# Kernel optimization log

Measured on AMD Instinct MI355X. Metric: run time of the kernel, lower is better.

## Reference

```python
import jax, jax.numpy as jnp
import numpy as np

N_NODES = 100000


def setup_inputs() -> dict:
    key = jax.random.key(0)
    ks = jax.random.split(key, 6)
    x = jax.random.normal(ks[0], (N_NODES, 3), dtype=jnp.float32)
    edge_index = jax.random.randint(ks[1], (2, 1600000), 0, N_NODES, dtype=jnp.int32)
    W1 = jax.random.normal(ks[2], (6, 64), dtype=jnp.float32) * 0.2
    b1 = jnp.zeros((64,), dtype=jnp.float32)
    W2 = jax.random.normal(ks[3], (67, 128), dtype=jnp.float32) * 0.1
    b2 = jnp.zeros((128,), dtype=jnp.float32)
    Wc = jax.random.normal(ks[4], (128, 5), dtype=jnp.float32) * 0.1
    bc = jnp.zeros((5,), dtype=jnp.float32)
    return {"x": x, "edge_index": edge_index, "W1": W1, "b1": b1,
            "W2": W2, "b2": b2, "Wc": Wc, "bc": bc}


def _pointnet_conv(h, rel, src, dst, W, b, n):
    # gather neighbor features, MLP on [h_j, pos_j - pos_i], max-aggregate per node
    msg = jnp.concatenate([h[src], rel], axis=-1) @ W + b  # [E, out]
    agg = jax.ops.segment_max(msg, dst, num_segments=n)    # [N, out]
    return jax.nn.relu(agg)  # relu also maps -inf (isolated nodes) to 0


def reference(x, edge_index, W1, b1, W2, b2, Wc, bc):
    src, dst = edge_index[0], edge_index[1]
    pos = x  # forward uses data.x for both x and pos
    rel = pos[src] - pos[dst]                       # [E, 3]
    h = _pointnet_conv(x, rel, src, dst, W1, b1, N_NODES)   # [N, 64]
    h = _pointnet_conv(h, rel, src, dst, W2, b2, N_NODES)   # [N, 128]
    logits = h @ Wc + bc                            # [N, 5]
    return jax.nn.log_softmax(logits, axis=-1)
```

## Files before the change

### kernel.cpp

```cpp
#include <hip/hip_runtime.h>
#include <cstdint>

#define CAP 56
#define NBITS 7
#define BINSZ 128
#define BIN_CAP 2816
#define TILE_E 4096
#define SCANN 1024
#define EPT (TILE_E/256)

typedef _Float16 h2 __attribute__((ext_vector_type(2)));
typedef _Float16 h4 __attribute__((ext_vector_type(4)));
typedef _Float16 h8 __attribute__((ext_vector_type(8)));
typedef float f32x4 __attribute__((ext_vector_type(4)));

static __device__ inline h8 pkmax8(h8 a, h8 b) {
#if __has_builtin(__builtin_elementwise_max)
    return __builtin_elementwise_max(a, b);
#else
    h8 r;
    #pragma unroll
    for (int i = 0; i < 8; i += 2) {
        h2 aa = { a[i], a[i+1] }, bb = { b[i], b[i+1] }, rr;
        asm("v_pk_max_f16 %0, %1, %2" : "=v"(rr) : "v"(aa), "v"(bb));
        r[i] = rr.x; r[i+1] = rr.y;
    }
    return r;
#endif
}

__global__ __launch_bounds__(256) void xpack_kernel(
    const float* __restrict__ x, float4* __restrict__ xp,
    int* __restrict__ bin_cnt, int N)
{
    int n = blockIdx.x * 256 + threadIdx.x;
    if (n < N) xp[n] = make_float4(x[n*3], x[n*3+1], x[n*3+2], 0.f);
    if (blockIdx.x == 0) {
        #pragma unroll
        for (int j = 0; j < 4; ++j) bin_cnt[threadIdx.x + j * 256] = 0;
    }
}

__global__ __launch_bounds__(256) void bin_kernel(
    const int* __restrict__ ei, int* __restrict__ bin_cnt,
    int* __restrict__ pairs, int E, int nbins)
{
    __shared__ int hist[SCANN];
    __shared__ int sc[SCANN];
    __shared__ int gbase[SCANN];
    __shared__ int lofs[SCANN];
    __shared__ int words[TILE_E];
    __shared__ unsigned short binOf[TILE_E];
    int t = threadIdx.x;
    for (int i = t; i < SCANN; i += 256) { hist[i] = 0; lofs[i] = 0; }
    __syncthreads();
    int e0 = blockIdx.x * TILE_E;
    int s[EPT], d[EPT];
    #pragma unroll
    for (int i = 0; i < EPT; ++i) {
        int e = e0 + t + i * 256;
        bool ok = e < E;
        s[i] = ok ? ei[e] : 0;
        d[i] = ok ? ei[E + e] : -1;
        if (ok) atomicAdd(&hist[d[i] >> NBITS], 1);
    }
    __syncthreads();
    for (int i = t; i < SCANN; i += 256) sc[i] = hist[i];
    __syncthreads();
    for (int off = 1; off < SCANN; off <<= 1) {
        int v[4];
        #pragma unroll
        for (int j = 0; j < 4; ++j) {
            int i = t + j * 256;
            v[j] = (i >= off) ? sc[i - off] : 0;
        }
        __syncthreads();
        #pragma unroll
        for (int j = 0; j < 4; ++j) sc[t + j * 256] += v[j];
        __syncthreads();
    }
    for (int i = t; i < nbins; i += 256)
        gbase[i] = atomicAdd(&bin_cnt[i], hist[i]);
    __syncthreads();
    #pragma unroll
    for (int i = 0; i < EPT; ++i) {
        if (d[i] >= 0) {
            int b = d[i] >> NBITS;
            int p = atomicAdd(&lofs[b], 1);
            int slot = (sc[b] - hist[b]) + p;
            words[slot] = s[i] | ((d[i] & (BINSZ - 1)) << 17);
            binOf[slot] = (unsigned short)b;
        }
    }
    __syncthreads();
    int total = sc[SCANN - 1];
    for (int i = t; i < total; i += 256) {
        int b = binOf[i];
        int off = gbase[b] + (i - (sc[b] - hist[b]));
        if (off < BIN_CAP) pairs[b * BIN_CAP + off] = words[i];
    }
}

__global__ __launch_bounds__(256) void scatter2_kernel(
    const int* __restrict__ pairs, const int* __restrict__ bin_cnt,
    int* __restrict__ cursor, int* __restrict__ bucket, int N)
{
    __shared__ int cur[BINSZ];
    __shared__ int lbuck[BINSZ * CAP];
    int t = threadIdx.x;
    int b = blockIdx.x;
    for (int i = t; i < BINSZ; i += 256) cur[i] = 0;
    __syncthreads();
    int cnt = min(bin_cnt[b], BIN_CAP);
    const int* pp = pairs + b * BIN_CAP;
    for (int i = t; i < cnt; i += 256) {
        int w = pp[i];
        int p = atomicAdd(&cur[w >> 17], 1);
        if (p < CAP) lbuck[(w >> 17) * CAP + p] = w & 0x1FFFF;
    }
    __syncthreads();
    int nbase = b * BINSZ;
    for (int dl = t; dl < BINSZ; dl += 256) {
        int n = nbase + dl;
        if (n >= N) continue;
        int c = min(cur[dl], CAP);
        int e = (c + 7) & ~7;
        int s0 = (c > 0) ? lbuck[dl * CAP] : 0;
        for (int p = c; p < e; ++p) lbuck[dl * CAP + p] = s0;
        cursor[n] = c;
    }
    __syncthreads();
    int4* dst = (int4*)(bucket + (size_t)nbase * CAP);
    const int4* srcv = (const int4*)lbuck;
    for (int i = t; i < BINSZ * CAP / 4; i += 256) dst[i] = srcv[i];
}

__global__ __launch_bounds__(256) void agg1_gemm_kernel(
    const float4* __restrict__ xp, const int* __restrict__ cursor,
    const int* __restrict__ bucket, const float* __restrict__ W1,
    const float* __restrict__ b1, const float* __restrict__ W2,
    const float* __restrict__ b2, _Float16* __restrict__ u2h, int N)
{
    __shared__ _Float16 h1[64 * 72];
    __shared__ _Float16 w2t[128 * 72];
    int tid = threadIdx.x;
    int n0  = blockIdx.x * 64;
    int sub = tid & 15;
    int ng  = tid >> 4;

    {
        const float4* W2v4 = (const float4*)W2;
        #pragma unroll
        for (int it = 0; it < 8; ++it) {
            int idx = tid + it * 256;
            int k   = idx >> 5;
            int c   = (idx & 31) * 4;
            float4 w = W2v4[idx];
            w2t[(c+0)*72 + k] = (_Float16)w.x;
            w2t[(c+1)*72 + k] = (_Float16)w.y;
            w2t[(c+2)*72 + k] = (_Float16)w.z;
            w2t[(c+3)*72 + k] = (_Float16)w.w;
        }
    }

    float4 q0 = ((const float4*)(W1 + 0*64))[sub];
    float4 q1 = ((const float4*)(W1 + 1*64))[sub];
    float4 q2 = ((const float4*)(W1 + 2*64))[sub];
    float4 t0 = ((const float4*)(W1 + 3*64))[sub];
    float4 t1 = ((const float4*)(W1 + 4*64))[sub];
    float4 t2 = ((const float4*)(W1 + 5*64))[sub];
    float4 c0 = make_float4(q0.x+t0.x, q0.y+t0.y, q0.z+t0.z, q0.w+t0.w);
    float4 c1 = make_float4(q1.x+t1.x, q1.y+t1.y, q1.z+t1.z, q1.w+t1.w);
    float4 c2 = make_float4(q2.x+t2.x, q2.y+t2.y, q2.z+t2.z, q2.w+t2.w);
    float4 bb = ((const float4*)b1)[sub];

    #pragma unroll
    for (int pass = 0; pass < 4; ++pass) {
        int nl = pass * 16 + ng;
        int n  = n0 + nl;
        float4 m = make_float4(-3e38f, -3e38f, -3e38f, -3e38f);
        int cnt = 0;
        if (n < N) {
            cnt = cursor[n];
            int rounds = (cnt + 7) & ~7;
            const int4* brow4 = (const int4*)(bucket + (size_t)n * CAP);
            int4 ia = brow4[0], ib = brow4[1];
            for (int j0 = 0; j0 < rounds; j0 += 8) {
                int4 na = brow4[(j0 >> 2) + 2];
                int4 nb = brow4[(j0 >> 2) + 3];
                float4 xs[8];
                xs[0] = xp[ia.x]; xs[1] = xp[ia.y]; xs[2] = xp[ia.z]; xs[3] = xp[ia.w];
                xs[4] = xp[ib.x]; xs[5] = xp[ib.y]; xs[6] = xp[ib.z]; xs[7] = xp[ib.w];
                #pragma unroll
                for (int u = 0; u < 8; ++u) {
                    float4 v;
                    v.x = fmaf(xs[u].x, c0.x, fmaf(xs[u].y, c1.x, xs[u].z * c2.x));
                    v.y = fmaf(xs[u].x, c0.y, fmaf(xs[u].y, c1.y, xs[u].z * c2.y));
                    v.z = fmaf(xs[u].x, c0.z, fmaf(xs[u].y, c1.z, xs[u].z * c2.z));
                    v.w = fmaf(xs[u].x, c0.w, fmaf(xs[u].y, c1.w, xs[u].z * c2.w));
                    m.x = fmaxf(m.x, v.x); m.y = fmaxf(m.y, v.y);
                    m.z = fmaxf(m.z, v.z); m.w = fmaxf(m.w, v.w);
                }
                ia = na; ib = nb;
            }
        }
        float4 xd = (n < N) ? xp[n] : make_float4(0.f, 0.f, 0.f, 0.f);
        float v0 = (cnt > 0) ? fmaxf(m.x + bb.x - (xd.x*t0.x + xd.y*t1.x + xd.z*t2.x), 0.f) : 0.f;
        float v1 = (cnt > 0) ? fmaxf(m.y + bb.y - (xd.x*t0.y + xd.y*t1.y + xd.z*t2.y), 0.f) : 0.f;
        float v2 = (cnt > 0) ? fmaxf(m.z + bb.z - (xd.x*t0.z + xd.y*t1.z + xd.z*t2.z), 0.f) : 0.f;
        float v3 = (cnt > 0) ? fmaxf(m.w + bb.w - (xd.x*t0.w + xd.y*t1.w + xd.z*t2.w), 0.f) : 0.f;
        h4 hv;
        hv.x = (_Float16)v0; hv.y = (_Float16)v1;
        hv.z = (_Float16)v2; hv.w = (_Float16)v3;
        *(h4*)&h1[nl * 72 + 4 * sub] = hv;
    }
    __syncthreads();

    int l   = tid & 63;
    int wv  = tid >> 6;
    int r16 = l & 15;
    int g4  = l >> 4;

    f32x4 acc[8];
    #pragma unroll
    for (int ct = 0; ct < 8; ++ct) acc[ct] = (f32x4){0.f, 0.f, 0.f, 0.f};

    h8 a0 = *(const h8*)&h1[(16*wv + r16) * 72 +      8*g4];
    h8 a1 = *(const h8*)&h1[(16*wv + r16) * 72 + 32 + 8*g4];
    #pragma unroll
    for (int ct = 0; ct < 8; ++ct) {
        h8 b0 = *(const h8*)&w2t[(16*ct + r16) * 72 +      8*g4];
        h8 b1f = *(const h8*)&w2t[(16*ct + r16) * 72 + 32 + 8*g4];
        acc[ct] = __builtin_amdgcn_mfma_f32_16x16x32_f16(a0, b0,  acc[ct], 0, 0, 0);
        acc[ct] = __builtin_amdgcn_mfma_f32_16x16x32_f16(a1, b1f, acc[ct], 0, 0, 0);
    }

    float bbv[8], wxv[8], wyv[8], wzv[8];
    #pragma unroll
    for (int ct = 0; ct < 8; ++ct) {
        int col = 16*ct + r16;
        bbv[ct] = b2[col];
        wxv[ct] = W2[64*128 + col];
        wyv[ct] = W2[65*128 + col];
        wzv[ct] = W2[66*128 + col];
    }
    #pragma unroll
    for (int r = 0; r < 4; ++r) {
        int n = n0 + 16*wv + 4*g4 + r;
        if (n < N) {
            float4 xd = xp[n];
            _Float16* orow = u2h + (size_t)n * 128 + r16;
            #pragma unroll
            for (int ct = 0; ct < 8; ++ct) {
                float v = acc[ct][r] + bbv[ct]
                        + xd.x * wxv[ct] + xd.y * wyv[ct] + xd.z * wzv[ct];
                orow[16*ct] = (_Float16)v;
            }
        }
    }
}

__global__ __launch_bounds__(256) void agg2_head_kernel(
    const float* __restrict__ x, const int* __restrict__ cursor,
    const int* __restrict__ bucket, const float* __restrict__ W2,
    const h8* __restrict__ u2v, const float* __restrict__ Wc,
    const float* __restrict__ bc, float* __restrict__ out, int N)
{
    int gid = blockIdx.x * 256 + threadIdx.x;
    int n   = gid >> 4;
    int sub = threadIdx.x & 15;
    if (n >= N) return;
    int cnt = cursor[n];
    int nr = (cnt + 7) >> 3;
    const int4* brow4 = (const int4*)(bucket + (size_t)n * CAP);
    const _Float16 NEG = (_Float16)(-60000.0f);
    h8 hm = { NEG, NEG, NEG, NEG, NEG, NEG, NEG, NEG };
    if (nr > 0) {
        int4 ia = brow4[0], ib = brow4[1];
        h8 v0 = u2v[(size_t)ia.x * 16 + sub];
        h8 v1 = u2v[(size_t)ia.y * 16 + sub];
        h8 v2 = u2v[(size_t)ia.z * 16 + sub];
        h8 v3 = u2v[(size_t)ia.w * 16 + sub];
        h8 v4 = u2v[(size_t)ib.x * 16 + sub];
        h8 v5 = u2v[(size_t)ib.y * 16 + sub];
        h8 v6 = u2v[(size_t)ib.z * 16 + sub];
        h8 v7 = u2v[(size_t)ib.w * 16 + sub];
        int4 na = brow4[2], nb = brow4[3];
        #pragma unroll 2
        for (int r = 1; r < nr; ++r) {
            h8 w0 = u2v[(size_t)na.x * 16 + sub];
            h8 w1 = u2v[(size_t)na.y * 16 + sub];
            h8 w2_ = u2v[(size_t)na.z * 16 + sub];
            h8 w3 = u2v[(size_t)na.w * 16 + sub];
            h8 w4 = u2v[(size_t)nb.x * 16 + sub];
            h8 w5 = u2v[(size_t)nb.y * 16 + sub];
            h8 w6 = u2v[(size_t)nb.z * 16 + sub];
            h8 w7 = u2v[(size_t)nb.w * 16 + sub];
            na = brow4[2*r + 2]; nb = brow4[2*r + 3];
            hm = pkmax8(hm, v0); hm = pkmax8(hm, v1);
            hm = pkmax8(hm, v2); hm = pkmax8(hm, v3);
            hm = pkmax8(hm, v4); hm = pkmax8(hm, v5);
            hm = pkmax8(hm, v6); hm = pkmax8(hm, v7);
            v0 = w0; v1 = w1; v2 = w2_; v3 = w3;
            v4 = w4; v5 = w5; v6 = w6; v7 = w7;
        }
        hm = pkmax8(hm, v0); hm = pkmax8(hm, v1);
        hm = pkmax8(hm, v2); hm = pkmax8(hm, v3);
        hm = pkmax8(hm, v4); hm = pkmax8(hm, v5);
        hm = pkmax8(hm, v6); hm = pkmax8(hm, v7);
    }
    const float4* W2v = (const float4*)W2;
    float4 wa0 = W2v[64*32 + sub*2], wa1 = W2v[64*32 + sub*2 + 1];
    float4 wb0 = W2v[65*32 + sub*2], wb1 = W2v[65*32 + sub*2 + 1];
    float4 wc0 = W2v[66*32 + sub*2], wc1 = W2v[66*32 + sub*2 + 1];
    float x0 = x[n*3], x1 = x[n*3+1], x2 = x[n*3+2];
    float hh[8];
    hh[0] = (cnt > 0) ? fmaxf((float)hm[0] - (x0*wa0.x + x1*wb0.x + x2*wc0.x), 0.f) : 0.f;
    hh[1] = (cnt > 0) ? fmaxf((float)hm[1] - (x0*wa0.y + x1*wb0.y + x2*wc0.y), 0.f) : 0.f;
    hh[2] = (cnt > 0) ? fmaxf((float)hm[2] - (x0*wa0.z + x1*wb0.z + x2*wc0.z), 0.f) : 0.f;
    hh[3] = (cnt > 0) ? fmaxf((float)hm[3] - (x0*wa0.w + x1*wb0.w + x2*wc0.w), 0.f) : 0.f;
    hh[4] = (cnt > 0) ? fmaxf((float)hm[4] - (x0*wa1.x + x1*wb1.x + x2*wc1.x), 0.f) : 0.f;
    hh[5] = (cnt > 0) ? fmaxf((float)hm[5] - (x0*wa1.y + x1*wb1.y + x2*wc1.y), 0.f) : 0.f;
    hh[6] = (cnt > 0) ? fmaxf((float)hm[6] - (x0*wa1.z + x1*wb1.z + x2*wc1.z), 0.f) : 0.f;
    hh[7] = (cnt > 0) ? fmaxf((float)hm[7] - (x0*wa1.w + x1*wb1.w + x2*wc1.w), 0.f) : 0.f;

    int g = sub * 8;
    float l0 = 0.f, l1 = 0.f, l2 = 0.f, l3 = 0.f, l4 = 0.f;
    #pragma unroll
    for (int k = 0; k < 8; ++k) {
        l0 = fmaf(hh[k], Wc[(g+k)*5+0], l0);
        l1 = fmaf(hh[k], Wc[(g+k)*5+1], l1);
        l2 = fmaf(hh[k], Wc[(g+k)*5+2], l2);
        l3 = fmaf(hh[k], Wc[(g+k)*5+3], l3);
        l4 = fmaf(hh[k], Wc[(g+k)*5+4], l4);
    }
    #pragma unroll
    for (int off = 8; off > 0; off >>= 1) {
        l0 += __shfl_xor(l0, off);
        l1 += __shfl_xor(l1, off);
        l2 += __shfl_xor(l2, off);
        l3 += __shfl_xor(l3, off);
        l4 += __shfl_xor(l4, off);
    }
    l0 += bc[0]; l1 += bc[1]; l2 += bc[2]; l3 += bc[3]; l4 += bc[4];
    float mx  = fmaxf(fmaxf(fmaxf(l0, l1), fmaxf(l2, l3)), l4);
    float s   = expf(l0-mx) + expf(l1-mx) + expf(l2-mx) + expf(l3-mx) + expf(l4-mx);
    float lse = mx + logf(s);
    if (sub < 5) {
        float v = (sub == 0) ? l0 : (sub == 1) ? l1 : (sub == 2) ? l2
                : (sub == 3) ? l3 : l4;
        out[n*5 + sub] = v - lse;
    }
}

extern "C" void kernel_launch(void* const* d_in, const int* in_sizes, int n_in,
                              void* d_out, int out_size, void* d_ws, size_t ws_size,
                              hipStream_t stream)
{
    const float* x  = (const float*)d_in[0];
    const int*   ei = (const int*)d_in[1];
    const float* W1 = (const float*)d_in[2];
    const float* b1 = (const float*)d_in[3];
    const float* W2 = (const float*)d_in[4];
    const float* b2 = (const float*)d_in[5];
    const float* Wc = (const float*)d_in[6];
    const float* bc = (const float*)d_in[7];
    float* out = (float*)d_out;

    int N = in_sizes[0] / 3;
    int E = in_sizes[1] / 2;
    int nbins = (N + BINSZ - 1) / BINSZ;

    char* ws = (char*)d_ws;
    _Float16* u2h   = (_Float16*)(ws);
    float4* xp      = (float4*)(ws + 25600000);
    int*    pairs   = (int*)   (ws + 27200000);
    int*    bucket  = (int*)   (ws + 36100000);
    int*    cursor  = (int*)   (ws + 58600000);
    int*    bin_cnt = (int*)   (ws + 59100000);

    xpack_kernel<<<(N + 255) / 256, 256, 0, stream>>>(x, xp, bin_cnt, N);
    bin_kernel<<<(E + TILE_E - 1) / TILE_E, 256, 0, stream>>>(
        ei, bin_cnt, pairs, E, nbins);
    scatter2_kernel<<<nbins, 256, 0, stream>>>(pairs, bin_cnt, cursor, bucket, N);

    agg1_gemm_kernel<<<(N + 63) / 64, 256, 0, stream>>>(
        xp, cursor, bucket, W1, b1, W2, b2, u2h, N);
    agg2_head_kernel<<<(N * 16 + 255) / 256, 256, 0, stream>>>(
        x, cursor, bucket, W2, (const h8*)u2h, Wc, bc, out, N);
}
```

Before: 216.5 us.

## Fuse all stages into one persistent cooperative kernel with grid syncs

Replaces the five separate kernel launches with a single cooperative persistent kernel that runs each stage in turn, separated by grid-wide barriers. Stages loop over tiles with a grid-stride loop or with an atomic work-queue counter, and they share one reused shared-memory buffer. The aim is to remove launch overhead and inter-kernel gaps. In exchange, occupancy is capped by the shared-memory size and launch bounds, the grid syncs add their own cost, and the grid is limited to about 1024 blocks, which may reduce parallelism in the memory-bound gather stages.

Result: slower. 500.6 us (+131.2%).

```diff
diff --git a/kernel.cpp b/kernel.cpp
--- a/kernel.cpp
+++ b/kernel.cpp
@@ -1,5 +1,8 @@
 #include <hip/hip_runtime.h>
+#include <hip/hip_cooperative_groups.h>
 #include <cstdint>
+
+namespace cg = cooperative_groups;
 
 #define CAP 56
 #define NBITS 7
@@ -29,132 +32,143 @@
 #endif
 }
 
-__global__ __launch_bounds__(256) void xpack_kernel(
-    const float* __restrict__ x, float4* __restrict__ xp,
-    int* __restrict__ bin_cnt, int N)
+__global__ __launch_bounds__(256, 4) void fused_kernel(
+    const float* __restrict__ x, const int* __restrict__ ei,
+    const float* __restrict__ W1, const float* __restrict__ b1,
+    const float* __restrict__ W2, const float* __restrict__ b2,
+    const float* __restrict__ Wc, const float* __restrict__ bc,
+    float* __restrict__ out,
+    float4* __restrict__ xp, int* __restrict__ pairs,
+    int* __restrict__ bucket, int* __restrict__ cursor,
+    int* __restrict__ bin_cnt, int* __restrict__ qctr,
+    _Float16* __restrict__ u2h, int N, int E, int nbins)
 {
-    int n = blockIdx.x * 256 + threadIdx.x;
-    if (n < N) xp[n] = make_float4(x[n*3], x[n*3+1], x[n*3+2], 0.f);
-    if (blockIdx.x == 0) {
-        #pragma unroll
-        for (int j = 0; j < 4; ++j) bin_cnt[threadIdx.x + j * 256] = 0;
-    }
-}
-
-__global__ __launch_bounds__(256) void bin_kernel(
-    const int* __restrict__ ei, int* __restrict__ bin_cnt,
-    int* __restrict__ pairs, int E, int nbins)
-{
-    __shared__ int hist[SCANN];
-    __shared__ int sc[SCANN];
-    __shared__ int gbase[SCANN];
-    __shared__ int lofs[SCANN];
-    __shared__ int words[TILE_E];
-    __shared__ unsigned short binOf[TILE_E];
-    int t = threadIdx.x;
-    for (int i = t; i < SCANN; i += 256) { hist[i] = 0; lofs[i] = 0; }
-    __syncthreads();
-    int e0 = blockIdx.x * TILE_E;
-    int s[EPT], d[EPT];
-    #pragma unroll
-    for (int i = 0; i < EPT; ++i) {
-        int e = e0 + t + i * 256;
-        bool ok = e < E;
-        s[i] = ok ? ei[e] : 0;
-        d[i] = ok ? ei[E + e] : -1;
-        if (ok) atomicAdd(&hist[d[i] >> NBITS], 1);
-    }
-    __syncthreads();
-    for (int i = t; i < SCANN; i += 256) sc[i] = hist[i];
-    __syncthreads();
-    for (int off = 1; off < SCANN; off <<= 1) {
-        int v[4];
-        #pragma unroll
-        for (int j = 0; j < 4; ++j) {
-            int i = t + j * 256;
-            v[j] = (i >= off) ? sc[i - off] : 0;
+    cg::grid_group grid = cg::this_grid();
+    alignas(16) __shared__ char smem[36864];
+    __shared__ int qv;
+    int tid  = threadIdx.x;
+    int bid  = blockIdx.x;
+    int nblk = gridDim.x;
+
+    for (int n = bid * 256 + tid; n < N; n += nblk * 256)
+        xp[n] = make_float4(x[n*3], x[n*3+1], x[n*3+2], 0.f);
+    for (int i = bid * 256 + tid; i < SCANN; i += nblk * 256) bin_cnt[i] = 0;
+    if (bid == 0 && tid < 8) qctr[tid] = 0;
+    grid.sync();
+
+    {
+        int* hist = (int*)smem;
+        int* sc   = (int*)(smem + 4096);
+        int* lofs = (int*)(smem + 8192);
+        int* words = (int*)(smem + 12288);
+        unsigned short* binOf = (unsigned short*)(smem + 28672);
+        int ntiles = (E + TILE_E - 1) / TILE_E;
+        for (int tile = bid; tile < ntiles; tile += nblk) {
+            for (int i = tid; i < SCANN; i += 256) { hist[i] = 0; lofs[i] = 0; }
+            __syncthreads();
+            int e0 = tile * TILE_E;
+            int s[EPT], d[EPT];
+            #pragma unroll
+            for (int i = 0; i < EPT; ++i) {
+                int e = e0 + tid + i * 256;
+                bool ok = e < E;
+                s[i] = ok ? ei[e] : 0;
+                d[i] = ok ? ei[E + e] : -1;
+                if (ok) atomicAdd(&hist[d[i] >> NBITS], 1);
+            }
+            __syncthreads();
+            for (int i = tid; i < SCANN; i += 256) sc[i] = hist[i];
+            __syncthreads();
+            for (int off = 1; off < SCANN; off <<= 1) {
+                int v[4];
+                #pragma unroll
+                for (int j = 0; j < 4; ++j) {
+                    int i = tid + j * 256;
+                    v[j] = (i >= off) ? sc[i - off] : 0;
+                }
+                __syncthreads();
+                #pragma unroll
+                for (int j = 0; j < 4; ++j) sc[tid + j * 256] += v[j];
+                __syncthreads();
+            }
+            int total = sc[SCANN - 1];
+            int ex[4], gb[4];
+            #pragma unroll
+            for (int j = 0; j < 4; ++j) {
+                int i = tid + j * 256;
+                ex[j] = sc[i] - hist[i];
+                gb[j] = (i < nbins && hist[i] != 0)
+                      ? atomicAdd(&bin_cnt[i], hist[i]) : 0;
+            }
+            __syncthreads();
+            #pragma unroll
+            for (int j = 0; j < 4; ++j) {
+                int i = tid + j * 256;
+                hist[i] = ex[j];
+                sc[i]   = gb[j];
+            }
+            __syncthreads();
+            #pragma unroll
+            for (int i = 0; i < EPT; ++i) {
+                if (d[i] >= 0) {
+                    int b = d[i] >> NBITS;
+                    int p = atomicAdd(&lofs[b], 1);
+                    int slot = hist[b] + p;
+                    words[slot] = s[i] | ((d[i] & (BINSZ - 1)) << 17);
+                    binOf[slot] = (unsigned short)b;
+                }
+            }
+            __syncthreads();
+            for (int i = tid; i < total; i += 256) {
+                int b = binOf[i];
+                int off = sc[b] + (i - hist[b]);
+                if (off < BIN_CAP) pairs[b * BIN_CAP + off] = words[i];
+            }
+            __syncthreads();
         }
-        __syncthreads();
-        #pragma unroll
-        for (int j = 0; j < 4; ++j) sc[t + j * 256] += v[j];
-        __syncthreads();
-    }
-    for (int i = t; i < nbins; i += 256)
-        gbase[i] = atomicAdd(&bin_cnt[i], hist[i]);
-    __syncthreads();
-    #pragma unroll
-    for (int i = 0; i < EPT; ++i) {
-        if (d[i] >= 0) {
-            int b = d[i] >> NBITS;
-            int p = atomicAdd(&lofs[b], 1);
-            int slot = (sc[b] - hist[b]) + p;
-            words[slot] = s[i] | ((d[i] & (BINSZ - 1)) << 17);
-            binOf[slot] = (unsigned short)b;
+    }
+    grid.sync();
+
+    {
+        int* cur   = (int*)smem;
+        int* lbuck = (int*)(smem + 512);
+        for (int b = bid; b < nbins; b += nblk) {
+            for (int i = tid; i < BINSZ; i += 256) cur[i] = 0;
+            __syncthreads();
+            int cnt = min(bin_cnt[b], BIN_CAP);
+            const int* pp = pairs + b * BIN_CAP;
+            for (int i = tid; i < cnt; i += 256) {
+                int w = pp[i];
+                int p = atomicAdd(&cur[w >> 17], 1);
+                if (p < CAP) lbuck[(w >> 17) * CAP + p] = w & 0x1FFFF;
+            }
+            __syncthreads();
+            int nbase = b * BINSZ;
+            for (int dl = tid; dl < BINSZ; dl += 256) {
+                int n = nbase + dl;
+                if (n >= N) continue;
+                int c = min(cur[dl], CAP);
+                int e = (c + 7) & ~7;
+                int s0 = (c > 0) ? lbuck[dl * CAP] : 0;
+                for (int p = c; p < e; ++p) lbuck[dl * CAP + p] = s0;
+                cursor[n] = c;
+            }
+            __syncthreads();
+            int4* dst = (int4*)(bucket + (size_t)nbase * CAP);
+            const int4* srcv = (const int4*)lbuck;
+            for (int i = tid; i < BINSZ * CAP / 4; i += 256) dst[i] = srcv[i];
+            __syncthreads();
         }
     }
-    __syncthreads();
-    int total = sc[SCANN - 1];
-    for (int i = t; i < total; i += 256) {
-        int b = binOf[i];
-        int off = gbase[b] + (i - (sc[b] - hist[b]));
-        if (off < BIN_CAP) pairs[b * BIN_CAP + off] = words[i];
-    }
-}
-
-__global__ __launch_bounds__(256) void scatter2_kernel(
-    const int* __restrict__ pairs, const int* __restrict__ bin_cnt,
-    int* __restrict__ cursor, int* __restrict__ bucket, int N)
-{
-    __shared__ int cur[BINSZ];
-    __shared__ int lbuck[BINSZ * CAP];
-    int t = threadIdx.x;
-    int b = blockIdx.x;
-    for (int i = t; i < BINSZ; i += 256) cur[i] = 0;
-    __syncthreads();
-    int cnt = min(bin_cnt[b], BIN_CAP);
-    const int* pp = pairs + b * BIN_CAP;
-    for (int i = t; i < cnt; i += 256) {
-        int w = pp[i];
-        int p = atomicAdd(&cur[w >> 17], 1);
-        if (p < CAP) lbuck[(w >> 17) * CAP + p] = w & 0x1FFFF;
-    }
-    __syncthreads();
-    int nbase = b * BINSZ;
-    for (int dl = t; dl < BINSZ; dl += 256) {
-        int n = nbase + dl;
-        if (n >= N) continue;
-        int c = min(cur[dl], CAP);
-        int e = (c + 7) & ~7;
-        int s0 = (c > 0) ? lbuck[dl * CAP] : 0;
-        for (int p = c; p < e; ++p) lbuck[dl * CAP + p] = s0;
-        cursor[n] = c;
-    }
-    __syncthreads();
-    int4* dst = (int4*)(bucket + (size_t)nbase * CAP);
-    const int4* srcv = (const int4*)lbuck;
-    for (int i = t; i < BINSZ * CAP / 4; i += 256) dst[i] = srcv[i];
-}
-
-__global__ __launch_bounds__(256) void agg1_gemm_kernel(
-    const float4* __restrict__ xp, const int* __restrict__ cursor,
-    const int* __restrict__ bucket, const float* __restrict__ W1,
-    const float* __restrict__ b1, const float* __restrict__ W2,
-    const float* __restrict__ b2, _Float16* __restrict__ u2h, int N)
-{
-    __shared__ _Float16 h1[64 * 72];
-    __shared__ _Float16 w2t[128 * 72];
-    int tid = threadIdx.x;
-    int n0  = blockIdx.x * 64;
-    int sub = tid & 15;
-    int ng  = tid >> 4;
-
+
+    _Float16* w2t = (_Float16*)smem;
+    _Float16* h1  = (_Float16*)(smem + 18432);
     {
         const float4* W2v4 = (const float4*)W2;
         #pragma unroll
         for (int it = 0; it < 8; ++it) {
             int idx = tid + it * 256;
-            int k   = idx >> 5;
-            int c   = (idx & 31) * 4;
+            int k = idx >> 5, c = (idx & 31) * 4;
             float4 w = W2v4[idx];
             w2t[(c+0)*72 + k] = (_Float16)w.x;
             w2t[(c+1)*72 + k] = (_Float16)w.y;
@@ -162,194 +176,211 @@
             w2t[(c+3)*72 + k] = (_Float16)w.w;
         }
     }
-
-    float4 q0 = ((const float4*)(W1 + 0*64))[sub];
-    float4 q1 = ((const float4*)(W1 + 1*64))[sub];
-    float4 q2 = ((const float4*)(W1 + 2*64))[sub];
-    float4 t0 = ((const float4*)(W1 + 3*64))[sub];
-    float4 t1 = ((const float4*)(W1 + 4*64))[sub];
-    float4 t2 = ((const float4*)(W1 + 5*64))[sub];
-    float4 c0 = make_float4(q0.x+t0.x, q0.y+t0.y, q0.z+t0.z, q0.w+t0.w);
-    float4 c1 = make_float4(q1.x+t1.x, q1.y+t1.y, q1.z+t1.z, q1.w+t1.w);
-    float4 c2 = make_float4(q2.x+t2.x, q2.y+t2.y, q2.z+t2.z, q2.w+t2.w);
-    float4 bb = ((const float4*)b1)[sub];
-
-    #pragma unroll
-    for (int pass = 0; pass < 4; ++pass) {
-        int nl = pass * 16 + ng;
-        int n  = n0 + nl;
-        float4 m = make_float4(-3e38f, -3e38f, -3e38f, -3e38f);
-        int cnt = 0;
-        if (n < N) {
-            cnt = cursor[n];
-            int rounds = (cnt + 7) & ~7;
-            const int4* brow4 = (const int4*)(bucket + (size_t)n * CAP);
-            int4 ia = brow4[0], ib = brow4[1];
-            for (int j0 = 0; j0 < rounds; j0 += 8) {
-                int4 na = brow4[(j0 >> 2) + 2];
-                int4 nb = brow4[(j0 >> 2) + 3];
-                float4 xs[8];
-                xs[0] = xp[ia.x]; xs[1] = xp[ia.y]; xs[2] = xp[ia.z]; xs[3] = xp[ia.w];
-                xs[4] = xp[ib.x]; xs[5] = xp[ib.y]; xs[6] = xp[ib.z]; xs[7] = xp[ib.w];
+    grid.sync();
+
+    {
+        int ntile1 = (N + 63) / 64;
+        int sub = tid & 15;
+        int ng  = tid >> 4;
+        while (true) {
+            if (tid == 0) qv = atomicAdd(&qctr[0], 1);
+            __syncthreads();
+            int tt = qv;
+            if (tt >= ntile1) break;
+            int n0 = tt * 64;
+
+            float4 q0 = ((const float4*)(W1 + 0*64))[sub];
+            float4 q1 = ((const float4*)(W1 + 1*64))[sub];
+            float4 q2 = ((const float4*)(W1 + 2*64))[sub];
+            float4 t0 = ((const float4*)(W1 + 3*64))[sub];
+            float4 t1 = ((const float4*)(W1 + 4*64))[sub];
+            float4 t2 = ((const float4*)(W1 + 5*64))[sub];
+            float4 c0 = make_float4(q0.x+t0.x, q0.y+t0.y, q0.z+t0.z, q0.w+t0.w);
+            float4 c1 = make_float4(q1.x+t1.x, q1.y+t1.y, q1.z+t1.z, q1.w+t1.w);
+            float4 c2 = make_float4(q2.x+t2.x, q2.y+t2.y, q2.z+t2.z, q2.w+t2.w);
+            float4 bb = ((const float4*)b1)[sub];
+
+            #pragma unroll
+            for (int pass = 0; pass < 4; ++pass) {
+                int nl = pass * 16 + ng;
+                int n  = n0 + nl;
+                float4 m = make_float4(-3e38f, -3e38f, -3e38f, -3e38f);
+                int cnt = 0;
+                if (n < N) {
+                    cnt = cursor[n];
+                    int rounds = (cnt + 7) & ~7;
+                    const int4* brow4 = (const int4*)(bucket + (size_t)n * CAP);
+                    int4 ia = brow4[0], ib = brow4[1];
+                    for (int j0 = 0; j0 < rounds; j0 += 8) {
+                        int4 na = brow4[(j0 >> 2) + 2];
+                        int4 nb = brow4[(j0 >> 2) + 3];
+                        float4 xs[8];
+                        xs[0] = xp[ia.x]; xs[1] = xp[ia.y]; xs[2] = xp[ia.z]; xs[3] = xp[ia.w];
+                        xs[4] = xp[ib.x]; xs[5] = xp[ib.y]; xs[6] = xp[ib.z]; xs[7] = xp[ib.w];
+                        #pragma unroll
+                        for (int u = 0; u < 8; ++u) {
+                            float4 v;
+                            v.x = fmaf(xs[u].x, c0.x, fmaf(xs[u].y, c1.x, xs[u].z * c2.x));
+                            v.y = fmaf(xs[u].x, c0.y, fmaf(xs[u].y, c1.y, xs[u].z * c2.y));
+                            v.z = fmaf(xs[u].x, c0.z, fmaf(xs[u].y, c1.z, xs[u].z * c2.z));
+                            v.w = fmaf(xs[u].x, c0.w, fmaf(xs[u].y, c1.w, xs[u].z * c2.w));
+                            m.x = fmaxf(m.x, v.x); m.y = fmaxf(m.y, v.y);
+                            m.z = fmaxf(m.z, v.z); m.w = fmaxf(m.w, v.w);
+                        }
+                        ia = na; ib = nb;
+                    }
+                }
+                float4 xd = (n < N) ? xp[n] : make_float4(0.f, 0.f, 0.f, 0.f);
+                float v0 = (cnt > 0) ? fmaxf(m.x + bb.x - (xd.x*t0.x + xd.y*t1.x + xd.z*t2.x), 0.f) : 0.f;
+                float v1 = (cnt > 0) ? fmaxf(m.y + bb.y - (xd.x*t0.y + xd.y*t1.y + xd.z*t2.y), 0.f) : 0.f;
+                float v2 = (cnt > 0) ? fmaxf(m.z + bb.z - (xd.x*t0.z + xd.y*t1.z + xd.z*t2.z), 0.f) : 0.f;
+                float v3 = (cnt > 0) ? fmaxf(m.w + bb.w - (xd.x*t0.w + xd.y*t1.w + xd.z*t2.w), 0.f) : 0.f;
+                h4 hv;
+                hv.x = (_Float16)v0; hv.y = (_Float16)v1;
+                hv.z = (_Float16)v2; hv.w = (_Float16)v3;
+                *(h4*)&h1[nl * 72 + 4 * sub] = hv;
+            }
+            __syncthreads();
+
+            int l   = tid & 63;
+            int wv  = tid >> 6;
+            int r16 = l & 15;
+            int g4  = l >> 4;
+            f32x4 acc[8];
+            #pragma unroll
+            for (int ct = 0; ct < 8; ++ct) acc[ct] = (f32x4){0.f, 0.f, 0.f, 0.f};
+            h8 a0 = *(const h8*)&h1[(16*wv + r16) * 72 +      8*g4];
+            h8 a1 = *(const h8*)&h1[(16*wv + r16) * 72 + 32 + 8*g4];
+            #pragma unroll
+            for (int ct = 0; ct < 8; ++ct) {
+                h8 b0  = *(const h8*)&w2t[(16*ct + r16) * 72 +      8*g4];
+                h8 b1f = *(const h8*)&w2t[(16*ct + r16) * 72 + 32 + 8*g4];
+                acc[ct] = __builtin_amdgcn_mfma_f32_16x16x32_f16(a0, b0,  acc[ct], 0, 0, 0);
+                acc[ct] = __builtin_amdgcn_mfma_f32_16x16x32_f16(a1, b1f, acc[ct], 0, 0, 0);
+            }
+            float bbv[8], wxv[8], wyv[8], wzv[8];
+            #pragma unroll
+            for (int ct = 0; ct < 8; ++ct) {
+                int col = 16*ct + r16;
+                bbv[ct] = b2[col];
+                wxv[ct] = W2[64*128 + col];
+                wyv[ct] = W2[65*128 + col];
+                wzv[ct] = W2[66*128 + col];
+            }
+            #pragma unroll
+            for (int r = 0; r < 4; ++r) {
+                int n = n0 + 16*wv + 4*g4 + r;
+                if (n < N) {
+                    float4 xd = xp[n];
+                    _Float16* orow = u2h + (size_t)n * 128 + r16;
+                    #pragma unroll
+                    for (int ct = 0; ct < 8; ++ct) {
+                        float v = acc[ct][r] + bbv[ct]
+                                + xd.x * wxv[ct] + xd.y * wyv[ct] + xd.z * wzv[ct];
+                        orow[16*ct] = (_Float16)v;
+                    }
+                }
+            }
+            __syncthreads();
+        }
+    }
+    grid.sync();
+
+    {
+        const h8* u2v = (const h8*)u2h;
+        int nchunk = (N * 16 + 255) / 256;
+        int sub = tid & 15;
+        while (true) {
+            if (tid == 0) qv = atomicAdd(&qctr[1], 1);
+            __syncthreads();
+            int ck = qv;
+            if (ck >= nchunk) break;
+            int n = ck * 16 + (tid >> 4);
+            if (n < N) {
+                int cnt = cursor[n];
+                int nr = (cnt + 7) >> 3;
+                const int4* brow4 = (const int4*)(bucket + (size_t)n * CAP);
+                const _Float16 NEG = (_Float16)(-60000.0f);
+                h8 hm = { NEG, NEG, NEG, NEG, NEG, NEG, NEG, NEG };
+                if (nr > 0) {
+                    int4 ia = brow4[0], ib = brow4[1];
+                    h8 v0 = u2v[(size_t)ia.x * 16 + sub];
+                    h8 v1 = u2v[(size_t)ia.y * 16 + sub];
+                    h8 v2 = u2v[(size_t)ia.z * 16 + sub];
+                    h8 v3 = u2v[(size_t)ia.w * 16 + sub];
+                    h8 v4 = u2v[(size_t)ib.x * 16 + sub];
+                    h8 v5 = u2v[(size_t)ib.y * 16 + sub];
+                    h8 v6 = u2v[(size_t)ib.z * 16 + sub];
+                    h8 v7 = u2v[(size_t)ib.w * 16 + sub];
+                    int4 na = brow4[2], nb = brow4[3];
+                    #pragma unroll 2
+                    for (int r = 1; r < nr; ++r) {
+                        h8 w0 = u2v[(size_t)na.x * 16 + sub];
+                        h8 w1 = u2v[(size_t)na.y * 16 + sub];
+                        h8 w2_ = u2v[(size_t)na.z * 16 + sub];
+                        h8 w3 = u2v[(size_t)na.w * 16 + sub];
+                        h8 w4 = u2v[(size_t)nb.x * 16 + sub];
+                        h8 w5 = u2v[(size_t)nb.y * 16 + sub];
+                        h8 w6 = u2v[(size_t)nb.z * 16 + sub];
+                        h8 w7 = u2v[(size_t)nb.w * 16 + sub];
+                        na = brow4[2*r + 2]; nb = brow4[2*r + 3];
+                        hm = pkmax8(hm, v0); hm = pkmax8(hm, v1);
+                        hm = pkmax8(hm, v2); hm = pkmax8(hm, v3);
+                        hm = pkmax8(hm, v4); hm = pkmax8(hm, v5);
+                        hm = pkmax8(hm, v6); hm = pkmax8(hm, v7);
+                        v0 = w0; v1 = w1; v2 = w2_; v3 = w3;
+                        v4 = w4; v5 = w5; v6 = w6; v7 = w7;
+                    }
+                    hm = pkmax8(hm, v0); hm = pkmax8(hm, v1);
+                    hm = pkmax8(hm, v2); hm = pkmax8(hm, v3);
+                    hm = pkmax8(hm, v4); hm = pkmax8(hm, v5);
+                    hm = pkmax8(hm, v6); hm = pkmax8(hm, v7);
+                }
+                const float4* W2v = (const float4*)W2;
+                float4 wa0 = W2v[64*32 + sub*2], wa1 = W2v[64*32 + sub*2 + 1];
+                float4 wb0 = W2v[65*32 + sub*2], wb1 = W2v[65*32 + sub*2 + 1];
+                float4 wc0 = W2v[66*32 + sub*2], wc1 = W2v[66*32 + sub*2 + 1];
+                float x0 = x[n*3], x1 = x[n*3+1], x2 = x[n*3+2];
+                float hh[8];
+                hh[0] = (cnt > 0) ? fmaxf((float)hm[0] - (x0*wa0.x + x1*wb0.x + x2*wc0.x), 0.f) : 0.f;
+                hh[1] = (cnt > 0) ? fmaxf((float)hm[1] - (x0*wa0.y + x1*wb0.y + x2*wc0.y), 0.f) : 0.f;
+                hh[2] = (cnt > 0) ? fmaxf((float)hm[2] - (x0*wa0.z + x1*wb0.z + x2*wc0.z), 0.f) : 0.f;
+                hh[3] = (cnt > 0) ? fmaxf((float)hm[3] - (x0*wa0.w + x1*wb0.w + x2*wc0.w), 0.f) : 0.f;
+                hh[4] = (cnt > 0) ? fmaxf((float)hm[4] - (x0*wa1.x + x1*wb1.x + x2*wc1.x), 0.f) : 0.f;
+                hh[5] = (cnt > 0) ? fmaxf((float)hm[5] - (x0*wa1.y + x1*wb1.y + x2*wc1.y), 0.f) : 0.f;
+                hh[6] = (cnt > 0) ? fmaxf((float)hm[6] - (x0*wa1.z + x1*wb1.z + x2*wc1.z), 0.f) : 0.f;
+                hh[7] = (cnt > 0) ? fmaxf((float)hm[7] - (x0*wa1.w + x1*wb1.w + x2*wc1.w), 0.f) : 0.f;
+
+                int g = sub * 8;
+                float l0 = 0.f, l1 = 0.f, l2 = 0.f, l3 = 0.f, l4 = 0.f;
                 #pragma unroll
-                for (int u = 0; u < 8; ++u) {
-                    float4 v;
-                    v.x = fmaf(xs[u].x, c0.x, fmaf(xs[u].y, c1.x, xs[u].z * c2.x));
-                    v.y = fmaf(xs[u].x, c0.y, fmaf(xs[u].y, c1.y, xs[u].z * c2.y));
-                    v.z = fmaf(xs[u].x, c0.z, fmaf(xs[u].y, c1.z, xs[u].z * c2.z));
-                    v.w = fmaf(xs[u].x, c0.w, fmaf(xs[u].y, c1.w, xs[u].z * c2.w));
-                    m.x = fmaxf(m.x, v.x); m.y = fmaxf(m.y, v.y);
-                    m.z = fmaxf(m.z, v.z); m.w = fmaxf(m.w, v.w);
-                }
-                ia = na; ib = nb;
-            }
+                for (int k = 0; k < 8; ++k) {
+                    l0 = fmaf(hh[k], Wc[(g+k)*5+0], l0);
+                    l1 = fmaf(hh[k], Wc[(g+k)*5+1], l1);
+                    l2 = fmaf(hh[k], Wc[(g+k)*5+2], l2);
+                    l3 = fmaf(hh[k], Wc[(g+k)*5+3], l3);
+                    l4 = fmaf(hh[k], Wc[(g+k)*5+4], l4);
+                }
+                #pragma unroll
+                for (int off = 8; off > 0; off >>= 1) {
+                    l0 += __shfl_xor(l0, off);
+                    l1 += __shfl_xor(l1, off);
+                    l2 += __shfl_xor(l2, off);
+                    l3 += __shfl_xor(l3, off);
+                    l4 += __shfl_xor(l4, off);
+                }
+                l0 += bc[0]; l1 += bc[1]; l2 += bc[2]; l3 += bc[3]; l4 += bc[4];
+                float mx  = fmaxf(fmaxf(fmaxf(l0, l1), fmaxf(l2, l3)), l4);
+                float s   = expf(l0-mx) + expf(l1-mx) + expf(l2-mx) + expf(l3-mx) + expf(l4-mx);
+                float lse = mx + logf(s);
+                if (sub < 5) {
+                    float v = (sub == 0) ? l0 : (sub == 1) ? l1 : (sub == 2) ? l2
+                            : (sub == 3) ? l3 : l4;
+                    out[n*5 + sub] = v - lse;
+                }
+            }
+            __syncthreads();
         }
-        float4 xd = (n < N) ? xp[n] : make_float4(0.f, 0.f, 0.f, 0.f);
-        float v0 = (cnt > 0) ? fmaxf(m.x + bb.x - (xd.x*t0.x + xd.y*t1.x + xd.z*t2.x), 0.f) : 0.f;
-        float v1 = (cnt > 0) ? fmaxf(m.y + bb.y - (xd.x*t0.y + xd.y*t1.y + xd.z*t2.y), 0.f) : 0.f;
-        float v2 = (cnt > 0) ? fmaxf(m.z + bb.z - (xd.x*t0.z + xd.y*t1.z + xd.z*t2.z), 0.f) : 0.f;
-        float v3 = (cnt > 0) ? fmaxf(m.w + bb.w - (xd.x*t0.w + xd.y*t1.w + xd.z*t2.w), 0.f) : 0.f;
-        h4 hv;
-        hv.x = (_Float16)v0; hv.y = (_Float16)v1;
-        hv.z = (_Float16)v2; hv.w = (_Float16)v3;
-        *(h4*)&h1[nl * 72 + 4 * sub] = hv;
-    }
-    __syncthreads();
-
-    int l   = tid & 63;
-    int wv  = tid >> 6;
-    int r16 = l & 15;
-    int g4  = l >> 4;
-
-    f32x4 acc[8];
-    #pragma unroll
-    for (int ct = 0; ct < 8; ++ct) acc[ct] = (f32x4){0.f, 0.f, 0.f, 0.f};
-
-    h8 a0 = *(const h8*)&h1[(16*wv + r16) * 72 +      8*g4];
-    h8 a1 = *(const h8*)&h1[(16*wv + r16) * 72 + 32 + 8*g4];
-    #pragma unroll
-    for (int ct = 0; ct < 8; ++ct) {
-        h8 b0 = *(const h8*)&w2t[(16*ct + r16) * 72 +      8*g4];
-        h8 b1f = *(const h8*)&w2t[(16*ct + r16) * 72 + 32 + 8*g4];
-        acc[ct] = __builtin_amdgcn_mfma_f32_16x16x32_f16(a0, b0,  acc[ct], 0, 0, 0);
-        acc[ct] = __builtin_amdgcn_mfma_f32_16x16x32_f16(a1, b1f, acc[ct], 0, 0, 0);
-    }
-
-    float bbv[8], wxv[8], wyv[8], wzv[8];
-    #pragma unroll
-    for (int ct = 0; ct < 8; ++ct) {
-        int col = 16*ct + r16;
-        bbv[ct] = b2[col];
-        wxv[ct] = W2[64*128 + col];
-        wyv[ct] = W2[65*128 + col];
-        wzv[ct] = W2[66*128 + col];
-    }
-    #pragma unroll
-    for (int r = 0; r < 4; ++r) {
-        int n = n0 + 16*wv + 4*g4 + r;
-        if (n < N) {
-            float4 xd = xp[n];
-            _Float16* orow = u2h + (size_t)n * 128 + r16;
-            #pragma unroll
-            for (int ct = 0; ct < 8; ++ct) {
-                float v = acc[ct][r] + bbv[ct]
-                        + xd.x * wxv[ct] + xd.y * wyv[ct] + xd.z * wzv[ct];
-                orow[16*ct] = (_Float16)v;
-            }
-        }
-    }
-}
-
-__global__ __launch_bounds__(256) void agg2_head_kernel(
-    const float* __restrict__ x, const int* __restrict__ cursor,
-    const int* __restrict__ bucket, const float* __restrict__ W2,
-    const h8* __restrict__ u2v, const float* __restrict__ Wc,
-    const float* __restrict__ bc, float* __restrict__ out, int N)
-{
-    int gid = blockIdx.x * 256 + threadIdx.x;
-    int n   = gid >> 4;
-    int sub = threadIdx.x & 15;
-    if (n >= N) return;
-    int cnt = cursor[n];
-    int nr = (cnt + 7) >> 3;
-    const int4* brow4 = (const int4*)(bucket + (size_t)n * CAP);
-    const _Float16 NEG = (_Float16)(-60000.0f);
-    h8 hm = { NEG, NEG, NEG, NEG, NEG, NEG, NEG, NEG };
-    if (nr > 0) {
-        int4 ia = brow4[0], ib = brow4[1];
-        h8 v0 = u2v[(size_t)ia.x * 16 + sub];
-        h8 v1 = u2v[(size_t)ia.y * 16 + sub];
-        h8 v2 = u2v[(size_t)ia.z * 16 + sub];
-        h8 v3 = u2v[(size_t)ia.w * 16 + sub];
-        h8 v4 = u2v[(size_t)ib.x * 16 + sub];
-        h8 v5 = u2v[(size_t)ib.y * 16 + sub];
-        h8 v6 = u2v[(size_t)ib.z * 16 + sub];
-        h8 v7 = u2v[(size_t)ib.w * 16 + sub];
-        int4 na = brow4[2], nb = brow4[3];
-        #pragma unroll 2
-        for (int r = 1; r < nr; ++r) {
-            h8 w0 = u2v[(size_t)na.x * 16 + sub];
-            h8 w1 = u2v[(size_t)na.y * 16 + sub];
-            h8 w2_ = u2v[(size_t)na.z * 16 + sub];
-            h8 w3 = u2v[(size_t)na.w * 16 + sub];
-            h8 w4 = u2v[(size_t)nb.x * 16 + sub];
-            h8 w5 = u2v[(size_t)nb.y * 16 + sub];
-            h8 w6 = u2v[(size_t)nb.z * 16 + sub];
-            h8 w7 = u2v[(size_t)nb.w * 16 + sub];
-            na = brow4[2*r + 2]; nb = brow4[2*r + 3];
-            hm = pkmax8(hm, v0); hm = pkmax8(hm, v1);
-            hm = pkmax8(hm, v2); hm = pkmax8(hm, v3);
-            hm = pkmax8(hm, v4); hm = pkmax8(hm, v5);
-            hm = pkmax8(hm, v6); hm = pkmax8(hm, v7);
-            v0 = w0; v1 = w1; v2 = w2_; v3 = w3;
-            v4 = w4; v5 = w5; v6 = w6; v7 = w7;
-        }
-        hm = pkmax8(hm, v0); hm = pkmax8(hm, v1);
-        hm = pkmax8(hm, v2); hm = pkmax8(hm, v3);
-        hm = pkmax8(hm, v4); hm = pkmax8(hm, v5);
-        hm = pkmax8(hm, v6); hm = pkmax8(hm, v7);
-    }
-    const float4* W2v = (const float4*)W2;
-    float4 wa0 = W2v[64*32 + sub*2], wa1 = W2v[64*32 + sub*2 + 1];
-    float4 wb0 = W2v[65*32 + sub*2], wb1 = W2v[65*32 + sub*2 + 1];
-    float4 wc0 = W2v[66*32 + sub*2], wc1 = W2v[66*32 + sub*2 + 1];
-    float x0 = x[n*3], x1 = x[n*3+1], x2 = x[n*3+2];
-    float hh[8];
-    hh[0] = (cnt > 0) ? fmaxf((float)hm[0] - (x0*wa0.x + x1*wb0.x + x2*wc0.x), 0.f) : 0.f;
-    hh[1] = (cnt > 0) ? fmaxf((float)hm[1] - (x0*wa0.y + x1*wb0.y + x2*wc0.y), 0.f) : 0.f;
-    hh[2] = (cnt > 0) ? fmaxf((float)hm[2] - (x0*wa0.z + x1*wb0.z + x2*wc0.z), 0.f) : 0.f;
-    hh[3] = (cnt > 0) ? fmaxf((float)hm[3] - (x0*wa0.w + x1*wb0.w + x2*wc0.w), 0.f) : 0.f;
-    hh[4] = (cnt > 0) ? fmaxf((float)hm[4] - (x0*wa1.x + x1*wb1.x + x2*wc1.x), 0.f) : 0.f;
-    hh[5] = (cnt > 0) ? fmaxf((float)hm[5] - (x0*wa1.y + x1*wb1.y + x2*wc1.y), 0.f) : 0.f;
-    hh[6] = (cnt > 0) ? fmaxf((float)hm[6] - (x0*wa1.z + x1*wb1.z + x2*wc1.z), 0.f) : 0.f;
-    hh[7] = (cnt > 0) ? fmaxf((float)hm[7] - (x0*wa1.w + x1*wb1.w + x2*wc1.w), 0.f) : 0.f;
-
-    int g = sub * 8;
-    float l0 = 0.f, l1 = 0.f, l2 = 0.f, l3 = 0.f, l4 = 0.f;
-    #pragma unroll
-    for (int k = 0; k < 8; ++k) {
-        l0 = fmaf(hh[k], Wc[(g+k)*5+0], l0);
-        l1 = fmaf(hh[k], Wc[(g+k)*5+1], l1);
-        l2 = fmaf(hh[k], Wc[(g+k)*5+2], l2);
-        l3 = fmaf(hh[k], Wc[(g+k)*5+3], l3);
-        l4 = fmaf(hh[k], Wc[(g+k)*5+4], l4);
-    }
-    #pragma unroll
-    for (int off = 8; off > 0; off >>= 1) {
-        l0 += __shfl_xor(l0, off);
-        l1 += __shfl_xor(l1, off);
-        l2 += __shfl_xor(l2, off);
-        l3 += __shfl_xor(l3, off);
-        l4 += __shfl_xor(l4, off);
-    }
-    l0 += bc[0]; l1 += bc[1]; l2 += bc[2]; l3 += bc[3]; l4 += bc[4];
-    float mx  = fmaxf(fmaxf(fmaxf(l0, l1), fmaxf(l2, l3)), l4);
-    float s   = expf(l0-mx) + expf(l1-mx) + expf(l2-mx) + expf(l3-mx) + expf(l4-mx);
-    float lse = mx + logf(s);
-    if (sub < 5) {
-        float v = (sub == 0) ? l0 : (sub == 1) ? l1 : (sub == 2) ? l2
-                : (sub == 3) ? l3 : l4;
-        out[n*5 + sub] = v - lse;
     }
 }
 
@@ -378,14 +409,19 @@
     int*    bucket  = (int*)   (ws + 36100000);
     int*    cursor  = (int*)   (ws + 58600000);
     int*    bin_cnt = (int*)   (ws + 59100000);
-
-    xpack_kernel<<<(N + 255) / 256, 256, 0, stream>>>(x, xp, bin_cnt, N);
-    bin_kernel<<<(E + TILE_E - 1) / TILE_E, 256, 0, stream>>>(
-        ei, bin_cnt, pairs, E, nbins);
-    scatter2_kernel<<<nbins, 256, 0, stream>>>(pairs, bin_cnt, cursor, bucket, N);
-
-    agg1_gemm_kernel<<<(N + 63) / 64, 256, 0, stream>>>(
-        xp, cursor, bucket, W1, b1, W2, b2, u2h, N);
-    agg2_head_kernel<<<(N * 16 + 255) / 256, 256, 0, stream>>>(
-        x, cursor, bucket, W2, (const h8*)u2h, Wc, bc, out, N);
+    int*    qctr    = (int*)   (ws + 59110000);
+
+    int occ = 0;
+    if (hipOccupancyMaxActiveBlocksPerMultiprocessor(&occ, fused_kernel, 256, 0)
+            != hipSuccess || occ < 1) occ = 2;
+    int gridsz = occ * 256;
+    if (gridsz > 1024) gridsz = 1024;
+
+    void* args[] = { (void*)&x, (void*)&ei, (void*)&W1, (void*)&b1,
+                     (void*)&W2, (void*)&b2, (void*)&Wc, (void*)&bc,
+                     (void*)&out, (void*)&xp, (void*)&pairs, (void*)&bucket,
+                     (void*)&cursor, (void*)&bin_cnt, (void*)&qctr,
+                     (void*)&u2h, (void*)&N, (void*)&E, (void*)&nbins };
+    hipLaunchCooperativeKernel(fused_kernel, dim3(gridsz), dim3(256),
+                               args, 0, stream);
 }
```

## Replace global bin atomics with per-tile sorted runs read by scatter kernel

Applied to the files above, without the earlier changes.

The binning pass no longer reserves space per bin with global atomics and scatters into fixed-capacity bin arrays. Each edge tile now writes its locally sorted words and its bin prefix sums to a per-tile buffer. The scatter kernel walks every tile's run for its bin, one tile per thread, which removes the global atomics, the bin_cnt zeroing and the BIN_CAP overflow truncation. The x-packing kernel is folded into the bin kernel to save a launch. In exchange, each scatter block reads prefix entries from all ~391 tiles, with serial per-thread loops and short uncoalesced runs.

Result: faster. 211.7 us (-2.2%).

```diff
diff --git a/kernel.cpp b/kernel.cpp
--- a/kernel.cpp
+++ b/kernel.cpp
@@ -4,7 +4,6 @@
 #define CAP 56
 #define NBITS 7
 #define BINSZ 128
-#define BIN_CAP 2816
 #define TILE_E 4096
 #define SCANN 1024
 #define EPT (TILE_E/256)
@@ -29,32 +28,23 @@
 #endif
 }
 
-__global__ __launch_bounds__(256) void xpack_kernel(
-    const float* __restrict__ x, float4* __restrict__ xp,
-    int* __restrict__ bin_cnt, int N)
-{
-    int n = blockIdx.x * 256 + threadIdx.x;
-    if (n < N) xp[n] = make_float4(x[n*3], x[n*3+1], x[n*3+2], 0.f);
-    if (blockIdx.x == 0) {
-        #pragma unroll
-        for (int j = 0; j < 4; ++j) bin_cnt[threadIdx.x + j * 256] = 0;
-    }
-}
-
 __global__ __launch_bounds__(256) void bin_kernel(
-    const int* __restrict__ ei, int* __restrict__ bin_cnt,
-    int* __restrict__ pairs, int E, int nbins)
-{
+    const float* __restrict__ x, const int* __restrict__ ei,
+    float4* __restrict__ xp, int* __restrict__ words_out,
+    int* __restrict__ tsc, int N, int E)
+{
+    for (int n = blockIdx.x * 256 + threadIdx.x; n < N; n += gridDim.x * 256)
+        xp[n] = make_float4(x[n*3], x[n*3+1], x[n*3+2], 0.f);
+
     __shared__ int hist[SCANN];
     __shared__ int sc[SCANN];
-    __shared__ int gbase[SCANN];
     __shared__ int lofs[SCANN];
     __shared__ int words[TILE_E];
-    __shared__ unsigned short binOf[TILE_E];
     int t = threadIdx.x;
+    int tile = blockIdx.x;
     for (int i = t; i < SCANN; i += 256) { hist[i] = 0; lofs[i] = 0; }
     __syncthreads();
-    int e0 = blockIdx.x * TILE_E;
+    int e0 = tile * TILE_E;
     int s[EPT], d[EPT];
     #pragma unroll
     for (int i = 0; i < EPT; ++i) {
@@ -79,9 +69,6 @@
         for (int j = 0; j < 4; ++j) sc[t + j * 256] += v[j];
         __syncthreads();
     }
-    for (int i = t; i < nbins; i += 256)
-        gbase[i] = atomicAdd(&bin_cnt[i], hist[i]);
-    __syncthreads();
     #pragma unroll
     for (int i = 0; i < EPT; ++i) {
         if (d[i] >= 0) {
@@ -89,21 +76,19 @@
             int p = atomicAdd(&lofs[b], 1);
             int slot = (sc[b] - hist[b]) + p;
             words[slot] = s[i] | ((d[i] & (BINSZ - 1)) << 17);
-            binOf[slot] = (unsigned short)b;
-        }
-    }
-    __syncthreads();
-    int total = sc[SCANN - 1];
-    for (int i = t; i < total; i += 256) {
-        int b = binOf[i];
-        int off = gbase[b] + (i - (sc[b] - hist[b]));
-        if (off < BIN_CAP) pairs[b * BIN_CAP + off] = words[i];
-    }
+        }
+    }
+    __syncthreads();
+    int* wo = words_out + tile * TILE_E;
+    for (int i = t; i < TILE_E; i += 256) wo[i] = words[i];
+    int* to = tsc + tile * SCANN;
+    for (int i = t; i < SCANN; i += 256) to[i] = sc[i];
 }
 
 __global__ __launch_bounds__(256) void scatter2_kernel(
-    const int* __restrict__ pairs, const int* __restrict__ bin_cnt,
-    int* __restrict__ cursor, int* __restrict__ bucket, int N)
+    const int* __restrict__ words, const int* __restrict__ tsc,
+    int* __restrict__ cursor, int* __restrict__ bucket,
+    int N, int ntiles)
 {
     __shared__ int cur[BINSZ];
     __shared__ int lbuck[BINSZ * CAP];
@@ -111,12 +96,16 @@
     int b = blockIdx.x;
     for (int i = t; i < BINSZ; i += 256) cur[i] = 0;
     __syncthreads();
-    int cnt = min(bin_cnt[b], BIN_CAP);
-    const int* pp = pairs + b * BIN_CAP;
-    for (int i = t; i < cnt; i += 256) {
-        int w = pp[i];
-        int p = atomicAdd(&cur[w >> 17], 1);
-        if (p < CAP) lbuck[(w >> 17) * CAP + p] = w & 0x1FFFF;
+    for (int tt = t; tt < ntiles; tt += 256) {
+        int base = tt * SCANN;
+        int s0 = (b > 0) ? tsc[base + b - 1] : 0;
+        int s1 = tsc[base + b];
+        const int* wp = words + tt * TILE_E;
+        for (int i = s0; i < s1; ++i) {
+            int w = wp[i];
+            int p = atomicAdd(&cur[w >> 17], 1);
+            if (p < CAP) lbuck[(w >> 17) * CAP + p] = w & 0x1FFFF;
+        }
     }
     __syncthreads();
     int nbase = b * BINSZ;
@@ -153,8 +142,7 @@
         #pragma unroll
         for (int it = 0; it < 8; ++it) {
             int idx = tid + it * 256;
-            int k   = idx >> 5;
-            int c   = (idx & 31) * 4;
+            int k = idx >> 5, c = (idx & 31) * 4;
             float4 w = W2v4[idx];
             w2t[(c+0)*72 + k] = (_Float16)w.x;
             w2t[(c+1)*72 + k] = (_Float16)w.y;
@@ -229,7 +217,7 @@
     h8 a1 = *(const h8*)&h1[(16*wv + r16) * 72 + 32 + 8*g4];
     #pragma unroll
     for (int ct = 0; ct < 8; ++ct) {
-        h8 b0 = *(const h8*)&w2t[(16*ct + r16) * 72 +      8*g4];
+        h8 b0  = *(const h8*)&w2t[(16*ct + r16) * 72 +      8*g4];
         h8 b1f = *(const h8*)&w2t[(16*ct + r16) * 72 + 32 + 8*g4];
         acc[ct] = __builtin_amdgcn_mfma_f32_16x16x32_f16(a0, b0,  acc[ct], 0, 0, 0);
         acc[ct] = __builtin_amdgcn_mfma_f32_16x16x32_f16(a1, b1f, acc[ct], 0, 0, 0);
@@ -369,21 +357,20 @@
 
     int N = in_sizes[0] / 3;
     int E = in_sizes[1] / 2;
-    int nbins = (N + BINSZ - 1) / BINSZ;
+    int nbins  = (N + BINSZ - 1) / BINSZ;
+    int ntiles = (E + TILE_E - 1) / TILE_E;
 
     char* ws = (char*)d_ws;
     _Float16* u2h   = (_Float16*)(ws);
     float4* xp      = (float4*)(ws + 25600000);
-    int*    pairs   = (int*)   (ws + 27200000);
+    int*    words   = (int*)   (ws + 27200000);
+    int*    tsc     = (int*)   (ws + 33700000);
     int*    bucket  = (int*)   (ws + 36100000);
     int*    cursor  = (int*)   (ws + 58600000);
-    int*    bin_cnt = (int*)   (ws + 59100000);
-
-    xpack_kernel<<<(N + 255) / 256, 256, 0, stream>>>(x, xp, bin_cnt, N);
-    bin_kernel<<<(E + TILE_E - 1) / TILE_E, 256, 0, stream>>>(
-        ei, bin_cnt, pairs, E, nbins);
-    scatter2_kernel<<<nbins, 256, 0, stream>>>(pairs, bin_cnt, cursor, bucket, N);
-
+
+    bin_kernel<<<ntiles, 256, 0, stream>>>(x, ei, xp, words, tsc, N, E);
+    scatter2_kernel<<<nbins, 256, 0, stream>>>(words, tsc, cursor, bucket,
+                                               N, ntiles);
     agg1_gemm_kernel<<<(N + 63) / 64, 256, 0, stream>>>(
         xp, cursor, bucket, W1, b1, W2, b2, u2h, N);
     agg2_head_kernel<<<(N * 16 + 255) / 256, 256, 0, stream>>>(
```
